# Kernel tuning notes

Hardware: AMD Instinct MI355X
Metric: run time of the kernel (lower is better)

Reference implementation:

```python
import jax, jax.numpy as jnp
import numpy as np
from jax import lax

EPS = 1e-5
T, N, E = 10, 10000, 320000
C_IN, C_HID, C_OUT = 16, 32, 16


def _stgcn_layer(x, edge_index, edge_weight, tw, tb, gw, gb, gamma, beta):
    # x: [T, N, Cin] -> temporal conv over T per node
    xc = jnp.transpose(x, (1, 2, 0))  # [N, Cin, T]
    y = lax.conv_general_dilated(xc, tw, window_strides=(1,), padding=((1, 1),),
                                 dimension_numbers=("NCH", "OIH", "NCH"))
    y = y + tb[None, :, None]
    y = jnp.clip(y, -10.0, 10.0)
    # InstanceNorm1d (affine, biased var over time axis)
    mu = jnp.mean(y, axis=-1, keepdims=True)
    var = jnp.mean((y - mu) ** 2, axis=-1, keepdims=True)
    y = (y - mu) * lax.rsqrt(var + EPS) * gamma[None, :, None] + beta[None, :, None]
    y = jax.nn.relu(y)
    h = jnp.transpose(y, (0, 2, 1))  # [N, T, C]

    n = h.shape[0]
    # GCNConv normalization (identical at every timestep -> computed once)
    ewn = jax.nn.softmax(edge_weight)  # softmax over all E edges
    loop = jnp.arange(n, dtype=edge_index.dtype)
    row = jnp.concatenate([edge_index[0], loop])  # sources (+self loops)
    col = jnp.concatenate([edge_index[1], loop])  # destinations
    w = jnp.concatenate([ewn, jnp.ones((n,), dtype=ewn.dtype)])
    deg = jax.ops.segment_sum(w, col, num_segments=n)
    dinv = jnp.where(deg > 0, lax.rsqrt(jnp.maximum(deg, EPS * 0 + 1e-30)), 0.0)
    norm = dinv[row] * w * dinv[col]  # [E+N]

    hw = jnp.einsum("ntc,cd->ntd", h, gw)  # [N, T, C]
    msg = hw[row] * norm[:, None, None]     # [E+N, T, C] gather
    agg = jax.ops.segment_sum(msg, col, num_segments=n) + gb  # scatter-add
    out = jnp.clip(jax.nn.relu(agg), -10.0, 10.0)
    return jnp.transpose(out, (1, 0, 2))  # [T, N, C]


def setup_inputs() -> dict:
    key = jax.random.key(0)
    ks = jax.random.split(key, 16)
    inp = {
        "x": jax.random.normal(ks[0], (T, N, C_IN), dtype=jnp.float32),
        "edge_index": jax.random.randint(ks[1], (2, E), 0, N, dtype=jnp.int32),
        "edge_weight": jax.random.uniform(ks[2], (E,), dtype=jnp.float32),
        # layer 1 (in -> hid)
        "l1_tw": jax.random.normal(ks[3], (C_HID, C_IN, 3), dtype=jnp.float32) * 0.02,
        "l1_tb": jnp.zeros((C_HID,), dtype=jnp.float32),
        "l1_gw": jax.random.normal(ks[4], (C_HID, C_HID), dtype=jnp.float32) * 0.1,
        "l1_gb": jnp.zeros((C_HID,), dtype=jnp.float32),
        "l1_gamma": jnp.ones((C_HID,), dtype=jnp.float32),
        "l1_beta": jnp.zeros((C_HID,), dtype=jnp.float32),
        # layer 2 (hid -> hid)
        "l2_tw": jax.random.normal(ks[5], (C_HID, C_HID, 3), dtype=jnp.float32) * 0.02,
        "l2_tb": jnp.zeros((C_HID,), dtype=jnp.float32),
        "l2_gw": jax.random.normal(ks[6], (C_HID, C_HID), dtype=jnp.float32) * 0.1,
        "l2_gb": jnp.zeros((C_HID,), dtype=jnp.float32),
        "l2_gamma": jnp.ones((C_HID,), dtype=jnp.float32),
        "l2_beta": jnp.zeros((C_HID,), dtype=jnp.float32),
        # output linear
        "out_w": jax.random.normal(ks[7], (C_HID, C_OUT), dtype=jnp.float32) * 0.1,
        "out_b": jnp.zeros((C_OUT,), dtype=jnp.float32),
    }
    return inp


def reference(x, edge_index, edge_weight,
              l1_tw, l1_tb, l1_gw, l1_gb, l1_gamma, l1_beta,
              l2_tw, l2_tb, l2_gw, l2_gb, l2_gamma, l2_beta,
              out_w, out_b):
    h = _stgcn_layer(x, edge_index, edge_weight, l1_tw, l1_tb, l1_gw, l1_gb, l1_gamma, l1_beta)
    h = _stgcn_layer(h, edge_index, edge_weight, l2_tw, l2_tb, l2_gw, l2_gb, l2_gamma, l2_beta)
    # per-timestep linear then mean over time == mean then linear, done faithfully
    outs = jnp.einsum("tnc,cd->tnd", h, out_w) + out_b
    return jnp.mean(outs, axis=0)  # [N, C_OUT]
```

## Files before the change

kernel.cpp:

```cpp
#include <hip/hip_runtime.h>
#include <hip/hip_bf16.h>
#include <string.h>


typedef __hip_bfloat16 bf16;

#define TSTEPS 10
#define TPAD 12
#define CHID 32
#define ROWELE (TSTEPS * CHID)
#define ROWW4 40

__device__ __forceinline__ float b2f(bf16 v) { return __bfloat162float(v); }
__device__ __forceinline__ float ldf(const void* p, long i, int bf) {
    return bf ? __bfloat162float(((const bf16*)p)[i]) : ((const float*)p)[i];
}
__device__ __forceinline__ int detect_bf(const unsigned* gbits) {
    return (gbits[0] != 0x3F800000u) ? 1 : 0;
}
__device__ __forceinline__ float bflo(unsigned u) { return __uint_as_float(u << 16); }
__device__ __forceinline__ float bfhi(unsigned u) { return __uint_as_float(u & 0xFFFF0000u); }
__device__ __forceinline__ unsigned pack2bf(float a, float b) {
    bf16 x = __float2bfloat16(a), y = __float2bfloat16(b);
    unsigned short ux, uy;
    memcpy(&ux, &x, 2); memcpy(&uy, &y, 2);
    return (unsigned)ux | ((unsigned)uy << 16);
}
__device__ __forceinline__ unsigned short bfbits(float a) {
    bf16 x = __float2bfloat16(a);
    unsigned short u; memcpy(&u, &x, 2);
    return u;
}
__device__ __forceinline__ void accum8(float* f, uint4 u, float w) {
    f[0] += w * bflo(u.x); f[1] += w * bfhi(u.x);
    f[2] += w * bflo(u.y); f[3] += w * bfhi(u.y);
    f[4] += w * bflo(u.z); f[5] += w * bfhi(u.z);
    f[6] += w * bflo(u.w); f[7] += w * bfhi(u.w);
}


__device__ __forceinline__ void edge_body(
    int bb, const void* __restrict__ ew, int bf, const int* __restrict__ ei,
    float* __restrict__ ewn, float* __restrict__ degx, int* __restrict__ cnt,
    float* __restrict__ sumexp, int E, int tid) {
    __shared__ float s_red[4];
    int i0 = (bb * 256 + tid) * 4;
    float e0 = 0.0f, e1 = 0.0f, e2 = 0.0f, e3 = 0.0f;
    if ((E & 3) == 0 && i0 + 3 < E) {
        float w0, w1, w2, w3;
        if (bf) {
            uint2 u = ((const uint2*)ew)[i0 >> 2];
            w0 = bflo(u.x); w1 = bfhi(u.x); w2 = bflo(u.y); w3 = bfhi(u.y);
        } else {
            float4 f = ((const float4*)ew)[i0 >> 2];
            w0 = f.x; w1 = f.y; w2 = f.z; w3 = f.w;
        }
        e0 = __expf(w0); e1 = __expf(w1); e2 = __expf(w2); e3 = __expf(w3);
        int4 c4 = *(const int4*)&ei[E + i0];
        atomicAdd(&degx[c4.x], e0); atomicAdd(&cnt[c4.x], 1);
        atomicAdd(&degx[c4.y], e1); atomicAdd(&cnt[c4.y], 1);
        atomicAdd(&degx[c4.z], e2); atomicAdd(&cnt[c4.z], 1);
        atomicAdd(&degx[c4.w], e3); atomicAdd(&cnt[c4.w], 1);
        *(float4*)&ewn[i0] = make_float4(e0, e1, e2, e3);
    } else {
        float es[4] = {0, 0, 0, 0};
        for (int j = 0; j < 4; j++) {
            int i = i0 + j;
            if (i < E) {
                float e = __expf(ldf(ew, i, bf));
                es[j] = e;
                ewn[i] = e;
                int c = ei[E + i];
                atomicAdd(&degx[c], e);
                atomicAdd(&cnt[c], 1);
            }
        }
        e0 = es[0]; e1 = es[1]; e2 = es[2]; e3 = es[3];
    }
    float v = (e0 + e1) + (e2 + e3);
    for (int o = 32; o > 0; o >>= 1) v += __shfl_down(v, o);
    int lane = tid & 63, wv = tid >> 6;
    if (lane == 0) s_red[wv] = v;
    __syncthreads();
    if (tid == 0) atomicAdd(sumexp, s_red[0] + s_red[1] + s_red[2] + s_red[3]);
}


template <int CIN, int LAYOUT>
__device__ __forceinline__ void conv_body(
    int bb, const void* __restrict__ in_, int bfw,
    const void* __restrict__ tw, const void* __restrict__ tb,
    const void* __restrict__ gamma, const void* __restrict__ beta,
    const void* __restrict__ gw,
    bf16* __restrict__ hw, int N, int tid) {
    constexpr int CO = CHID;
    __shared__ __align__(16) float s_in[8 * CIN * TPAD];
    __shared__ __align__(16) float s_h[8 * CO * TPAD];
    __shared__ __align__(16) unsigned s_tw01[CIN * CO];
    __shared__ __align__(16) unsigned short s_tw2[CIN * CO];
    __shared__ __align__(16) unsigned s_gwp[(CO / 2) * CO];

    int nl = tid >> 5, o = tid & 31;

    float tbv = ldf(tb, o, bfw);
    float gav = ldf(gamma, o, bfw);
    float bev = ldf(beta, o, bfw);

    for (int i = tid; i < CIN * CO; i += 256) {
        int ci = i / CO, oo = i % CO;
        long base = ((long)oo * CIN + ci) * 3;
        float w0 = ldf(tw, base, bfw);
        float w1 = ldf(tw, base + 1, bfw);
        float w2 = ldf(tw, base + 2, bfw);
        s_tw01[ci * CO + oo] = pack2bf(w0, w1);
        s_tw2[ci * CO + oo] = bfbits(w2);
    }
    for (int i = tid; i < (CO / 2) * CO; i += 256) {
        int cp = i / CO, oo = i % CO;
        s_gwp[i] = pack2bf(ldf(gw, (long)(2 * cp) * CO + oo, bfw),
                           ldf(gw, (long)(2 * cp + 1) * CO + oo, bfw));
    }

    int nb = bb * 8;

    if (LAYOUT == 0) {
        constexpr int CP = CIN / 2;
        for (int i2 = tid; i2 < 8 * TSTEPS * CP; i2 += 256) {
            int cp = i2 % CP;
            int t = (i2 / CP) % TSTEPS;
            int nn = i2 / (CP * TSTEPS);
            int n = nb + nn;
            float v0 = 0.0f, v1 = 0.0f;
            if (n < N) {
                long idx = (long)t * ((long)N * CIN) + (long)n * CIN + 2 * cp;
                if (bfw) {
                    unsigned u = ((const unsigned*)in_)[idx >> 1];
                    v0 = bflo(u); v1 = bfhi(u);
                } else {
                    float2 f = ((const float2*)in_)[idx >> 1];
                    v0 = f.x; v1 = f.y;
                }
            }
            int b = nn * (CIN * TPAD) + (2 * cp) * TPAD + t;
            s_in[b] = v0;
            s_in[b + TPAD] = v1;
        }
    } else {
        for (int i2 = tid; i2 < 8 * CIN * 5; i2 += 256) {
            int tp = i2 % 5;
            int ci = (i2 / 5) % CIN;
            int nn = i2 / (5 * CIN);
            int n = nb + nn;
            float v0 = 0.0f, v1 = 0.0f;
            if (n < N) {
                long idx = (long)n * (CIN * TSTEPS) + ci * TSTEPS + 2 * tp;
                unsigned u = ((const unsigned*)in_)[idx >> 1];
                v0 = bflo(u); v1 = bfhi(u);
            }
            int b = nn * (CIN * TPAD) + ci * TPAD + 2 * tp;
            s_in[b] = v0;
            s_in[b + 1] = v1;
        }
    }
    __syncthreads();

    int n = nb + nl;
    const float* xrow = &s_in[nl * CIN * TPAD];

    float acc[TSTEPS];
#pragma unroll
    for (int t = 0; t < TSTEPS; t++) acc[t] = tbv;

    for (int ci = 0; ci < CIN; ci++) {
        const float4* xp = (const float4*)&xrow[ci * TPAD];
        float4 A = xp[0], B = xp[1], C = xp[2];
        float xr[TSTEPS] = {A.x, A.y, A.z, A.w, B.x, B.y, B.z, B.w, C.x, C.y};
        unsigned w01 = s_tw01[ci * CO + o];
        float w0 = bflo(w01), w1 = bfhi(w01);
        float w2 = __uint_as_float(((unsigned)s_tw2[ci * CO + o]) << 16);
        acc[0] += xr[0] * w1 + xr[1] * w2;
#pragma unroll
        for (int t = 1; t < TSTEPS - 1; t++)
            acc[t] += xr[t - 1] * w0 + xr[t] * w1 + xr[t + 1] * w2;
        acc[TSTEPS - 1] += xr[TSTEPS - 2] * w0 + xr[TSTEPS - 1] * w1;
    }

#pragma unroll
    for (int t = 0; t < TSTEPS; t++) acc[t] = fminf(fmaxf(acc[t], -10.0f), 10.0f);
    float mu = 0.0f;
#pragma unroll
    for (int t = 0; t < TSTEPS; t++) mu += acc[t];
    mu *= 0.1f;
    float var = 0.0f;
#pragma unroll
    for (int t = 0; t < TSTEPS; t++) { float d = acc[t] - mu; var += d * d; }
    var *= 0.1f;
    float sc = gav * rsqrtf(var + 1e-5f);
    float h[TSTEPS];
#pragma unroll
    for (int t = 0; t < TSTEPS; t++) h[t] = fmaxf((acc[t] - mu) * sc + bev, 0.0f);

    float4* hp = (float4*)&s_h[nl * CO * TPAD + o * TPAD];
    hp[0] = make_float4(h[0], h[1], h[2], h[3]);
    hp[1] = make_float4(h[4], h[5], h[6], h[7]);
    hp[2] = make_float4(h[8], h[9], 0.0f, 0.0f);
    __syncthreads();

    float acc2[TSTEPS];
#pragma unroll
    for (int t = 0; t < TSTEPS; t++) acc2[t] = 0.0f;
    const float* hrow = &s_h[nl * CO * TPAD];
    for (int cp = 0; cp < CO / 2; cp++) {
        unsigned g2 = s_gwp[cp * CO + o];
        float g0 = bflo(g2), g1 = bfhi(g2);
        const float4* r0 = (const float4*)&hrow[(2 * cp) * TPAD];
        const float4* r1 = (const float4*)&hrow[(2 * cp + 1) * TPAD];
        float4 A0 = r0[0], B0 = r0[1], C0 = r0[2];
        float4 A1 = r1[0], B1 = r1[1], C1 = r1[2];
        acc2[0] += A0.x * g0 + A1.x * g1;
        acc2[1] += A0.y * g0 + A1.y * g1;
        acc2[2] += A0.z * g0 + A1.z * g1;
        acc2[3] += A0.w * g0 + A1.w * g1;
        acc2[4] += B0.x * g0 + B1.x * g1;
        acc2[5] += B0.y * g0 + B1.y * g1;
        acc2[6] += B0.z * g0 + B1.z * g1;
        acc2[7] += B0.w * g0 + B1.w * g1;
        acc2[8] += C0.x * g0 + C1.x * g1;
        acc2[9] += C0.y * g0 + C1.y * g1;
    }
    if (n < N) {
        unsigned* hwp = (unsigned*)hw;
        long base = (long)n * (ROWELE / 2) + o * (TSTEPS / 2);
#pragma unroll
        for (int j = 0; j < 5; j++)
            hwp[base + j] = pack2bf(acc2[2 * j], acc2[2 * j + 1]);
    }
}


__global__ __launch_bounds__(256) void edge_conv1_kernel(
    const void* __restrict__ ew, const unsigned* __restrict__ gbits,
    const int* __restrict__ ei,
    float* __restrict__ ewn, float* __restrict__ degx, int* __restrict__ cnt,
    float* __restrict__ sumexp, int E, int gE4,
    const void* __restrict__ x,
    const void* __restrict__ tw, const void* __restrict__ tb,
    const void* __restrict__ gamma, const void* __restrict__ beta,
    const void* __restrict__ gw,
    bf16* __restrict__ hw, int N) {
    int bf = detect_bf(gbits);
    int tid = threadIdx.x;
    if ((int)blockIdx.x < gE4) {
        edge_body(blockIdx.x, ew, bf, ei, ewn, degx, cnt, sumexp, E, tid);
    } else {
        conv_body<16, 0>(blockIdx.x - gE4, x, bf, tw, tb, gamma, beta, gw,
                         hw, N, tid);
    }
}

__global__ __launch_bounds__(256) void conv2_kernel(
    const void* __restrict__ in_, const unsigned* __restrict__ gbits,
    const void* __restrict__ tw, const void* __restrict__ tb,
    const void* __restrict__ gamma, const void* __restrict__ beta,
    const void* __restrict__ gw,
    bf16* __restrict__ hw, int N) {
    conv_body<32, 1>(blockIdx.x, in_, detect_bf(gbits), tw, tb, gamma, beta,
                     gw, hw, N, threadIdx.x);
}

__global__ __launch_bounds__(1024) void scan_kernel(const int* __restrict__ cnt,
                                                    const float* __restrict__ degx,
                                                    const float* __restrict__ sumexp,
                                                    float* __restrict__ dinv,
                                                    int* __restrict__ off, int N) {
    __shared__ int s[1024];
    int tid = threadIdx.x;
    float invS = 1.0f / (*sumexp);
    for (int i = tid; i < N; i += 1024) dinv[i] = rsqrtf(1.0f + degx[i] * invS);
    int chunk = (N + 1023) / 1024;
    int b0 = tid * chunk;
    int p = 0;
    for (int k = 0; k < chunk; k++) { int i = b0 + k; if (i < N) p += cnt[i]; }
    s[tid] = p;
    __syncthreads();
    for (int d = 1; d < 1024; d <<= 1) {
        int v = (tid >= d) ? s[tid - d] : 0;
        __syncthreads();
        s[tid] += v;
        __syncthreads();
    }
    int base = s[tid] - p;
    for (int k = 0; k < chunk; k++) {
        int i = b0 + k;
        if (i < N) {
            off[i] = base;
            base += cnt[i];
            if (i == N - 1) off[N] = base;
        }
    }
}


__global__ __launch_bounds__(256) void fill_kernel(const int* __restrict__ ei,
                                                   const float* __restrict__ ewn,
                                                   const float* __restrict__ dinv,
                                                   const float* __restrict__ sumexp,
                                                   const int* __restrict__ off,
                                                   int* __restrict__ cursor,
                                                   int2* __restrict__ csr, int E) {
    int i0 = (blockIdx.x * 256 + threadIdx.x) * 4;
    if (i0 >= E) return;
    float invS = 1.0f / (*sumexp);
    if ((E & 3) == 0 && i0 + 3 < E) {
        int4 r4 = *(const int4*)&ei[i0];
        int4 c4 = *(const int4*)&ei[E + i0];
        float4 e4 = *(const float4*)&ewn[i0];
        int rr[4] = {r4.x, r4.y, r4.z, r4.w};
        int cc[4] = {c4.x, c4.y, c4.z, c4.w};
        float ee[4] = {e4.x, e4.y, e4.z, e4.w};
#pragma unroll
        for (int j = 0; j < 4; j++) {
            int r = rr[j], c = cc[j];
            int p = atomicAdd(&cursor[c], 1);
            float w = dinv[r] * (ee[j] * invS) * dinv[c];
            csr[off[c] + p] = make_int2(r, __float_as_int(w));
        }
    } else {
        for (int j = 0; j < 4; j++) {
            int i = i0 + j;
            if (i >= E) break;
            int r = ei[i], c = ei[E + i];
            int p = atomicAdd(&cursor[c], 1);
            float w = dinv[r] * (ewn[i] * invS) * dinv[c];
            csr[off[c] + p] = make_int2(r, __float_as_int(w));
        }
    }
}


template <bool FINAL>
__global__ __launch_bounds__(320) void agg_kernel_t(
    const uint4* __restrict__ hw4, const int* __restrict__ off,
    const int2* __restrict__ csr,
    const float* __restrict__ dinv, const void* __restrict__ gb,
    const void* __restrict__ ow, const void* __restrict__ ob,
    const unsigned* __restrict__ gbits,
    void* __restrict__ out, int N) {
    __shared__ int2 s_sw[ROWELE];
    __shared__ float s_part[8 * ROWW4 * 9];
    __shared__ float s_hbar[CHID];
    __shared__ float s_ow[CHID * 16];
    __shared__ float s_ob[16];

    int bf = detect_bf(gbits);
    int n = blockIdx.x;
    int tid = threadIdx.x;
    int g = tid % ROWW4;
    int eo = tid / ROWW4;

    if (FINAL) {
        for (int i = tid; i < CHID * 16; i += ROWELE) s_ow[i] = ldf(ow, i, bf);
        if (tid < 16) s_ob[tid] = ldf(ob, tid, bf);
    }

    float facc[8];
#pragma unroll
    for (int j = 0; j < 8; j++) facc[j] = 0.0f;

    float dn = dinv[n];
    if (eo == 0) {
        uint4 u = hw4[n * ROWW4 + g];
        accum8(facc, u, dn * dn);
    }

    int beg = off[n], end = off[n + 1];
    for (int base = beg; base < end; base += ROWELE) {
        int m = min(ROWELE, end - base);
        if (tid < m) s_sw[tid] = csr[base + tid];
        __syncthreads();
        int kmax = (m + 7) >> 3;
        int k = 0;
        for (; k + 2 <= kmax; k += 2) {
            int j0 = (k << 3) + eo, j1 = j0 + 8;
            int c0 = min(j0, m - 1), c1 = min(j1, m - 1);
            int2 e0 = s_sw[c0], e1 = s_sw[c1];
            float w0 = (j0 < m) ? __int_as_float(e0.y) : 0.0f;
            float w1 = (j1 < m) ? __int_as_float(e1.y) : 0.0f;
            uint4 u0 = hw4[e0.x * ROWW4 + g];
            uint4 u1 = hw4[e1.x * ROWW4 + g];
            accum8(facc, u0, w0);
            accum8(facc, u1, w1);
        }
        if (k < kmax) {
            int j0 = (k << 3) + eo;
            int c0 = min(j0, m - 1);
            int2 e0 = s_sw[c0];
            float w0 = (j0 < m) ? __int_as_float(e0.y) : 0.0f;
            uint4 u0 = hw4[e0.x * ROWW4 + g];
            accum8(facc, u0, w0);
        }
        __syncthreads();
    }

    {
        float* rowp = &s_part[(eo * ROWW4 + g) * 9];
#pragma unroll
        for (int j = 0; j < 8; j++) rowp[j] = facc[j];
    }
    __syncthreads();
    int gg = tid >> 3, jj = tid & 7;
    float v = 0.0f;
#pragma unroll
    for (int s = 0; s < 8; s++) v += s_part[(s * ROWW4 + gg) * 9 + jj];
    int c = tid / TSTEPS;
    v += ldf(gb, c, bf);
    v = fminf(fmaxf(v, 0.0f), 10.0f);

    if (!FINAL) {
        ((bf16*)out)[(long)n * ROWELE + tid] = __float2bfloat16(v);
    } else {
        __syncthreads();
        s_part[tid] = v;
        __syncthreads();
        if (tid < CHID) {
            float s = 0.0f;
#pragma unroll
            for (int t = 0; t < TSTEPS; t++) s += s_part[tid * TSTEPS + t];
            s_hbar[tid] = s * 0.1f;
        }
        __syncthreads();
        if (tid < 16) {
            float a = s_ob[tid];
#pragma unroll
            for (int cc = 0; cc < CHID; cc++) a += s_hbar[cc] * s_ow[cc * 16 + tid];
            long oi = (long)n * 16 + tid;
            if (bf) ((bf16*)out)[oi] = __float2bfloat16(a);
            else    ((float*)out)[oi] = a;
        }
    }
}


extern "C" void kernel_launch(void* const* d_in, const int* in_sizes, int n_in,
                              void* d_out, int out_size, void* d_ws, size_t ws_size,
                              hipStream_t stream) {
    (void)n_in; (void)out_size; (void)ws_size;

    const void* x     = d_in[0];
    const int*  ei    = (const int*)d_in[1];
    const void* ew    = d_in[2];
    const void* l1_tw = d_in[3];
    const void* l1_tb = d_in[4];
    const void* l1_gw = d_in[5];
    const void* l1_gb = d_in[6];
    const unsigned* gbits = (const unsigned*)d_in[7];
    const void* l1_ga = d_in[7];
    const void* l1_be = d_in[8];
    const void* l2_tw = d_in[9];
    const void* l2_tb = d_in[10];
    const void* l2_gw = d_in[11];
    const void* l2_gb = d_in[12];
    const void* l2_ga = d_in[13];
    const void* l2_be = d_in[14];
    const void* out_w = d_in[15];
    const void* out_b = d_in[16];

    int N = in_sizes[0] / (TSTEPS * 16);
    int E = in_sizes[1] / 2;

    char* p = (char*)d_ws;
    auto alloc = [&](size_t bytes) -> char* {
        char* r = p;
        p += (bytes + 255) & ~(size_t)255;
        return r;
    };
    char* zbase   = p;
    float* sumexp = (float*)alloc(256);
    float* degx   = (float*)alloc((size_t)N * 4);
    int*   cnt    = (int*)alloc((size_t)N * 4);
    int*   cursor = (int*)alloc((size_t)N * 4);
    size_t zbytes = (size_t)(p - zbase);
    float* ewn     = (float*)alloc((size_t)E * 4);
    float* dinv    = (float*)alloc((size_t)N * 4);
    int*   offA    = (int*)alloc((size_t)(N + 1) * 4);
    int2*  csr     = (int2*)alloc((size_t)E * 8);
    bf16*  bufA    = (bf16*)alloc((size_t)N * ROWELE * 2);
    bf16*  bufB    = (bf16*)alloc((size_t)N * ROWELE * 2);

    int gE4 = (E + 1023) / 1024;
    int gConv = (N + 7) / 8;

    hipMemsetAsync(zbase, 0, zbytes, stream);
    hipLaunchKernelGGL(edge_conv1_kernel, dim3(gE4 + gConv), dim3(256), 0, stream,
                       ew, gbits, ei, ewn, degx, cnt, sumexp, E, gE4,
                       x, l1_tw, l1_tb, l1_ga, l1_be, l1_gw, bufA, N);
    hipLaunchKernelGGL(scan_kernel, dim3(1), dim3(1024), 0, stream,
                       cnt, degx, sumexp, dinv, offA, N);
    hipLaunchKernelGGL(fill_kernel, dim3(gE4), dim3(256), 0, stream,
                       ei, ewn, dinv, sumexp, offA, cursor, csr, E);

    hipLaunchKernelGGL((agg_kernel_t<false>), dim3(N), dim3(ROWELE), 0, stream,
                       (const uint4*)bufA, offA, csr, dinv, l1_gb,
                       nullptr, nullptr, gbits, (void*)bufB, N);
    hipLaunchKernelGGL(conv2_kernel, dim3(gConv), dim3(256), 0, stream,
                       (const void*)bufB, gbits, l2_tw, l2_tb, l2_ga, l2_be,
                       l2_gw, bufA, N);
    hipLaunchKernelGGL((agg_kernel_t<true>), dim3(N), dim3(ROWELE), 0, stream,
                       (const uint4*)bufA, offA, csr, dinv, l2_gb,
                       out_w, out_b, gbits, d_out, N);
}
```

Before: 278.6 us.

## Fuse scan into last edge block and layer-2 conv into first aggregation

The separate single-block scan kernel is removed. The last-finishing edge block, detected with an atomic done counter and threadfences, now computes dinv and the CSR offsets with a 256-thread scan. The layer-1 aggregation and the layer-2 temporal conv, instance norm and GCN weight multiply are fused into one per-node kernel, so the intermediate bufB round trip and two launches go away. In exchange, every node block reloads the conv weights into shared memory, the fused kernel uses more shared memory, and the scan now runs on 256 threads instead of 1024.

New measurement: 538.7 us. 93.3% more time.

```diff
diff --git a/kernel.cpp b/kernel.cpp
--- a/kernel.cpp
+++ b/kernel.cpp
@@ -11,7 +11,6 @@
 #define ROWELE (TSTEPS * CHID)
 #define ROWW4 40
 
-__device__ __forceinline__ float b2f(bf16 v) { return __bfloat162float(v); }
 __device__ __forceinline__ float ldf(const void* p, long i, int bf) {
     return bf ? __bfloat162float(((const bf16*)p)[i]) : ((const float*)p)[i];
 }
@@ -42,8 +41,11 @@
 __device__ __forceinline__ void edge_body(
     int bb, const void* __restrict__ ew, int bf, const int* __restrict__ ei,
     float* __restrict__ ewn, float* __restrict__ degx, int* __restrict__ cnt,
-    float* __restrict__ sumexp, int E, int tid) {
+    float* __restrict__ sumexp, int E, int gE4, int* __restrict__ done,
+    float* __restrict__ dinv, int* __restrict__ off, int N, int tid) {
     __shared__ float s_red[4];
+    __shared__ int s_last;
+    __shared__ int s_scan[256];
     int i0 = (bb * 256 + tid) * 4;
     float e0 = 0.0f, e1 = 0.0f, e2 = 0.0f, e3 = 0.0f;
     if ((E & 3) == 0 && i0 + 3 < E) {
@@ -83,6 +85,41 @@
     if (lane == 0) s_red[wv] = v;
     __syncthreads();
     if (tid == 0) atomicAdd(sumexp, s_red[0] + s_red[1] + s_red[2] + s_red[3]);
+
+    __threadfence();
+    __syncthreads();
+    if (tid == 0) s_last = (atomicAdd(done, 1) == gE4 - 1) ? 1 : 0;
+    __syncthreads();
+    if (!s_last) return;
+
+    __threadfence();
+    float invS = 1.0f / atomicAdd(sumexp, 0.0f);
+    for (int i = tid; i < N; i += 256)
+        dinv[i] = rsqrtf(1.0f + atomicAdd(&degx[i], 0.0f) * invS);
+    int chunk = (N + 255) >> 8;
+    int b0 = tid * chunk;
+    int p = 0;
+    for (int k = 0; k < chunk; k++) {
+        int i = b0 + k;
+        if (i < N) p += atomicAdd(&cnt[i], 0);
+    }
+    s_scan[tid] = p;
+    __syncthreads();
+    for (int d = 1; d < 256; d <<= 1) {
+        int u = (tid >= d) ? s_scan[tid - d] : 0;
+        __syncthreads();
+        s_scan[tid] += u;
+        __syncthreads();
+    }
+    int base = s_scan[tid] - p;
+    for (int k = 0; k < chunk; k++) {
+        int i = b0 + k;
+        if (i < N) {
+            off[i] = base;
+            base += atomicAdd(&cnt[i], 0);
+            if (i == N - 1) off[N] = base;
+        }
+    }
 }
 
 
@@ -109,11 +146,8 @@
     for (int i = tid; i < CIN * CO; i += 256) {
         int ci = i / CO, oo = i % CO;
         long base = ((long)oo * CIN + ci) * 3;
-        float w0 = ldf(tw, base, bfw);
-        float w1 = ldf(tw, base + 1, bfw);
-        float w2 = ldf(tw, base + 2, bfw);
-        s_tw01[ci * CO + oo] = pack2bf(w0, w1);
-        s_tw2[ci * CO + oo] = bfbits(w2);
+        s_tw01[ci * CO + oo] = pack2bf(ldf(tw, base, bfw), ldf(tw, base + 1, bfw));
+        s_tw2[ci * CO + oo] = bfbits(ldf(tw, base + 2, bfw));
     }
     for (int i = tid; i < (CO / 2) * CO; i += 256) {
         int cp = i / CO, oo = i % CO;
@@ -122,45 +156,26 @@
     }
 
     int nb = bb * 8;
-
-    if (LAYOUT == 0) {
-        constexpr int CP = CIN / 2;
-        for (int i2 = tid; i2 < 8 * TSTEPS * CP; i2 += 256) {
-            int cp = i2 % CP;
-            int t = (i2 / CP) % TSTEPS;
-            int nn = i2 / (CP * TSTEPS);
-            int n = nb + nn;
-            float v0 = 0.0f, v1 = 0.0f;
-            if (n < N) {
-                long idx = (long)t * ((long)N * CIN) + (long)n * CIN + 2 * cp;
-                if (bfw) {
-                    unsigned u = ((const unsigned*)in_)[idx >> 1];
-                    v0 = bflo(u); v1 = bfhi(u);
-                } else {
-                    float2 f = ((const float2*)in_)[idx >> 1];
-                    v0 = f.x; v1 = f.y;
-                }
-            }
-            int b = nn * (CIN * TPAD) + (2 * cp) * TPAD + t;
-            s_in[b] = v0;
-            s_in[b + TPAD] = v1;
-        }
-    } else {
-        for (int i2 = tid; i2 < 8 * CIN * 5; i2 += 256) {
-            int tp = i2 % 5;
-            int ci = (i2 / 5) % CIN;
-            int nn = i2 / (5 * CIN);
-            int n = nb + nn;
-            float v0 = 0.0f, v1 = 0.0f;
-            if (n < N) {
-                long idx = (long)n * (CIN * TSTEPS) + ci * TSTEPS + 2 * tp;
+    constexpr int CP = CIN / 2;
+    for (int i2 = tid; i2 < 8 * TSTEPS * CP; i2 += 256) {
+        int cp = i2 % CP;
+        int t = (i2 / CP) % TSTEPS;
+        int nn = i2 / (CP * TSTEPS);
+        int n = nb + nn;
+        float v0 = 0.0f, v1 = 0.0f;
+        if (n < N) {
+            long idx = (long)t * ((long)N * CIN) + (long)n * CIN + 2 * cp;
+            if (bfw) {
                 unsigned u = ((const unsigned*)in_)[idx >> 1];
                 v0 = bflo(u); v1 = bfhi(u);
+            } else {
+                float2 f = ((const float2*)in_)[idx >> 1];
+                v0 = f.x; v1 = f.y;
             }
-            int b = nn * (CIN * TPAD) + ci * TPAD + 2 * tp;
-            s_in[b] = v0;
-            s_in[b + 1] = v1;
-        }
+        }
+        int b = nn * (CIN * TPAD) + (2 * cp) * TPAD + t;
+        s_in[b] = v0;
+        s_in[b + TPAD] = v1;
     }
     __syncthreads();
 
@@ -237,12 +252,12 @@
     }
 }
 
-
 __global__ __launch_bounds__(256) void edge_conv1_kernel(
     const void* __restrict__ ew, const unsigned* __restrict__ gbits,
     const int* __restrict__ ei,
     float* __restrict__ ewn, float* __restrict__ degx, int* __restrict__ cnt,
-    float* __restrict__ sumexp, int E, int gE4,
+    float* __restrict__ sumexp, int E, int gE4, int* __restrict__ done,
+    float* __restrict__ dinv, int* __restrict__ off,
     const void* __restrict__ x,
     const void* __restrict__ tw, const void* __restrict__ tb,
     const void* __restrict__ gamma, const void* __restrict__ beta,
@@ -251,55 +266,13 @@
     int bf = detect_bf(gbits);
     int tid = threadIdx.x;
     if ((int)blockIdx.x < gE4) {
-        edge_body(blockIdx.x, ew, bf, ei, ewn, degx, cnt, sumexp, E, tid);
+        edge_body(blockIdx.x, ew, bf, ei, ewn, degx, cnt, sumexp, E, gE4,
+                  done, dinv, off, N, tid);
     } else {
         conv_body<16, 0>(blockIdx.x - gE4, x, bf, tw, tb, gamma, beta, gw,
                          hw, N, tid);
     }
 }
-
-__global__ __launch_bounds__(256) void conv2_kernel(
-    const void* __restrict__ in_, const unsigned* __restrict__ gbits,
-    const void* __restrict__ tw, const void* __restrict__ tb,
-    const void* __restrict__ gamma, const void* __restrict__ beta,
-    const void* __restrict__ gw,
-    bf16* __restrict__ hw, int N) {
-    conv_body<32, 1>(blockIdx.x, in_, detect_bf(gbits), tw, tb, gamma, beta,
-                     gw, hw, N, threadIdx.x);
-}
-
-__global__ __launch_bounds__(1024) void scan_kernel(const int* __restrict__ cnt,
-                                                    const float* __restrict__ degx,
-                                                    const float* __restrict__ sumexp,
-                                                    float* __restrict__ dinv,
-                                                    int* __restrict__ off, int N) {
-    __shared__ int s[1024];
-    int tid = threadIdx.x;
-    float invS = 1.0f / (*sumexp);
-    for (int i = tid; i < N; i += 1024) dinv[i] = rsqrtf(1.0f + degx[i] * invS);
-    int chunk = (N + 1023) / 1024;
-    int b0 = tid * chunk;
-    int p = 0;
-    for (int k = 0; k < chunk; k++) { int i = b0 + k; if (i < N) p += cnt[i]; }
-    s[tid] = p;
-    __syncthreads();
-    for (int d = 1; d < 1024; d <<= 1) {
-        int v = (tid >= d) ? s[tid - d] : 0;
-        __syncthreads();
-        s[tid] += v;
-        __syncthreads();
-    }
-    int base = s[tid] - p;
-    for (int k = 0; k < chunk; k++) {
-        int i = b0 + k;
-        if (i < N) {
-            off[i] = base;
-            base += cnt[i];
-            if (i == N - 1) off[N] = base;
-        }
-    }
-}
-
 
 __global__ __launch_bounds__(256) void fill_kernel(const int* __restrict__ ei,
                                                    const float* __restrict__ ewn,
@@ -338,30 +311,13 @@
 }
 
 
-template <bool FINAL>
-__global__ __launch_bounds__(320) void agg_kernel_t(
-    const uint4* __restrict__ hw4, const int* __restrict__ off,
-    const int2* __restrict__ csr,
-    const float* __restrict__ dinv, const void* __restrict__ gb,
-    const void* __restrict__ ow, const void* __restrict__ ob,
-    const unsigned* __restrict__ gbits,
-    void* __restrict__ out, int N) {
-    __shared__ int2 s_sw[ROWELE];
-    __shared__ float s_part[8 * ROWW4 * 9];
-    __shared__ float s_hbar[CHID];
-    __shared__ float s_ow[CHID * 16];
-    __shared__ float s_ob[16];
-
-    int bf = detect_bf(gbits);
-    int n = blockIdx.x;
-    int tid = threadIdx.x;
+__device__ __forceinline__ float agg_gather(
+    int n, int tid, const uint4* __restrict__ hw4, const int* __restrict__ off,
+    const int2* __restrict__ csr, const float* __restrict__ dinv,
+    const void* __restrict__ gb, int bf,
+    int2* s_sw, float* s_part) {
     int g = tid % ROWW4;
     int eo = tid / ROWW4;
-
-    if (FINAL) {
-        for (int i = tid; i < CHID * 16; i += ROWELE) s_ow[i] = ldf(ow, i, bf);
-        if (tid < 16) s_ob[tid] = ldf(ob, tid, bf);
-    }
 
     float facc[8];
 #pragma unroll
@@ -414,29 +370,157 @@
     for (int s = 0; s < 8; s++) v += s_part[(s * ROWW4 + gg) * 9 + jj];
     int c = tid / TSTEPS;
     v += ldf(gb, c, bf);
-    v = fminf(fmaxf(v, 0.0f), 10.0f);
-
-    if (!FINAL) {
-        ((bf16*)out)[(long)n * ROWELE + tid] = __float2bfloat16(v);
-    } else {
-        __syncthreads();
-        s_part[tid] = v;
-        __syncthreads();
-        if (tid < CHID) {
-            float s = 0.0f;
-#pragma unroll
-            for (int t = 0; t < TSTEPS; t++) s += s_part[tid * TSTEPS + t];
-            s_hbar[tid] = s * 0.1f;
-        }
-        __syncthreads();
-        if (tid < 16) {
-            float a = s_ob[tid];
-#pragma unroll
-            for (int cc = 0; cc < CHID; cc++) a += s_hbar[cc] * s_ow[cc * 16 + tid];
-            long oi = (long)n * 16 + tid;
-            if (bf) ((bf16*)out)[oi] = __float2bfloat16(a);
-            else    ((float*)out)[oi] = a;
-        }
+    return fminf(fmaxf(v, 0.0f), 10.0f);
+}
+
+
+__global__ __launch_bounds__(ROWELE) void agg1_conv2_kernel(
+    const uint4* __restrict__ hw4, const int* __restrict__ off,
+    const int2* __restrict__ csr,
+    const float* __restrict__ dinv, const void* __restrict__ gb,
+    const void* __restrict__ tw, const void* __restrict__ tb,
+    const void* __restrict__ gamma, const void* __restrict__ beta,
+    const void* __restrict__ gw,
+    const unsigned* __restrict__ gbits,
+    unsigned* __restrict__ hw2, int N) {
+    __shared__ int2 s_sw[ROWELE];
+    __shared__ float s_part[8 * ROWW4 * 9];
+    __shared__ float s_x[ROWELE];
+    __shared__ float s_y[ROWELE];
+    __shared__ float s_hh[ROWELE];
+    __shared__ unsigned s_tw01[CHID * CHID];
+    __shared__ unsigned short s_tw2[CHID * CHID];
+    __shared__ unsigned s_gwp[(CHID / 2) * CHID];
+    __shared__ float s_tb2[CHID], s_ga2[CHID], s_be2[CHID];
+    __shared__ float s_mu[CHID], s_sc[CHID];
+
+    int bf = detect_bf(gbits);
+    int n = blockIdx.x;
+    int tid = threadIdx.x;
+
+    for (int i = tid; i < CHID * CHID; i += ROWELE) {
+        int ci = i >> 5, o = i & 31;
+        long base = ((long)o * CHID + ci) * 3;
+        s_tw01[i] = pack2bf(ldf(tw, base, bf), ldf(tw, base + 1, bf));
+        s_tw2[i] = bfbits(ldf(tw, base + 2, bf));
+    }
+    for (int i = tid; i < (CHID / 2) * CHID; i += ROWELE) {
+        int cp = i >> 5, o = i & 31;
+        s_gwp[i] = pack2bf(ldf(gw, (long)(2 * cp) * CHID + o, bf),
+                           ldf(gw, (long)(2 * cp + 1) * CHID + o, bf));
+    }
+    if (tid < CHID) {
+        s_tb2[tid] = ldf(tb, tid, bf);
+        s_ga2[tid] = ldf(gamma, tid, bf);
+        s_be2[tid] = ldf(beta, tid, bf);
+    }
+
+    float v = agg_gather(n, tid, hw4, off, csr, dinv, gb, bf, s_sw, s_part);
+    s_x[tid] = v;
+    __syncthreads();
+
+    int o = tid / 5, j = tid % 5, t0 = 2 * j;
+    float y0 = 0.0f, y1 = 0.0f;
+    if (tid < 160) {
+        float a0 = s_tb2[o], a1 = a0;
+        for (int ci = 0; ci < CHID; ci++) {
+            const float* xb = &s_x[ci * TSTEPS];
+            float xm = (t0 > 0) ? xb[t0 - 1] : 0.0f;
+            float x0 = xb[t0];
+            float x1 = xb[t0 + 1];
+            float xp = (t0 < 8) ? xb[t0 + 2] : 0.0f;
+            unsigned w01 = s_tw01[ci * CHID + o];
+            float w0 = bflo(w01), w1 = bfhi(w01);
+            float w2 = __uint_as_float(((unsigned)s_tw2[ci * CHID + o]) << 16);
+            a0 += xm * w0 + x0 * w1 + x1 * w2;
+            a1 += x0 * w0 + x1 * w1 + xp * w2;
+        }
+        y0 = fminf(fmaxf(a0, -10.0f), 10.0f);
+        y1 = fminf(fmaxf(a1, -10.0f), 10.0f);
+        s_y[o * TSTEPS + t0] = y0;
+        s_y[o * TSTEPS + t0 + 1] = y1;
+    }
+    __syncthreads();
+
+    if (tid < CHID) {
+        const float* yb = &s_y[tid * TSTEPS];
+        float yv[TSTEPS];
+#pragma unroll
+        for (int t = 0; t < TSTEPS; t++) yv[t] = yb[t];
+        float mu = 0.0f;
+#pragma unroll
+        for (int t = 0; t < TSTEPS; t++) mu += yv[t];
+        mu *= 0.1f;
+        float var = 0.0f;
+#pragma unroll
+        for (int t = 0; t < TSTEPS; t++) { float d = yv[t] - mu; var += d * d; }
+        var *= 0.1f;
+        s_mu[tid] = mu;
+        s_sc[tid] = s_ga2[tid] * rsqrtf(var + 1e-5f);
+    }
+    __syncthreads();
+
+    if (tid < 160) {
+        float mu = s_mu[o], sc = s_sc[o], be = s_be2[o];
+        s_hh[o * TSTEPS + t0] = fmaxf((y0 - mu) * sc + be, 0.0f);
+        s_hh[o * TSTEPS + t0 + 1] = fmaxf((y1 - mu) * sc + be, 0.0f);
+    }
+    __syncthreads();
+
+    if (tid < 160) {
+        float a0 = 0.0f, a1 = 0.0f;
+        for (int cp = 0; cp < CHID / 2; cp++) {
+            unsigned g2 = s_gwp[cp * CHID + o];
+            float g0 = bflo(g2), g1 = bfhi(g2);
+            const float* h0 = &s_hh[(2 * cp) * TSTEPS];
+            const float* h1 = &s_hh[(2 * cp + 1) * TSTEPS];
+            a0 += h0[t0] * g0 + h1[t0] * g1;
+            a1 += h0[t0 + 1] * g0 + h1[t0 + 1] * g1;
+        }
+        hw2[(long)n * (ROWELE / 2) + tid] = pack2bf(a0, a1);
+    }
+}
+
+
+__global__ __launch_bounds__(ROWELE) void agg_final_kernel(
+    const uint4* __restrict__ hw4, const int* __restrict__ off,
+    const int2* __restrict__ csr,
+    const float* __restrict__ dinv, const void* __restrict__ gb,
+    const void* __restrict__ ow, const void* __restrict__ ob,
+    const unsigned* __restrict__ gbits,
+    void* __restrict__ out, int N) {
+    __shared__ int2 s_sw[ROWELE];
+    __shared__ float s_part[8 * ROWW4 * 9];
+    __shared__ float s_hbar[CHID];
+    __shared__ float s_ow[CHID * 16];
+    __shared__ float s_ob[16];
+
+    int bf = detect_bf(gbits);
+    int n = blockIdx.x;
+    int tid = threadIdx.x;
+
+    for (int i = tid; i < CHID * 16; i += ROWELE) s_ow[i] = ldf(ow, i, bf);
+    if (tid < 16) s_ob[tid] = ldf(ob, tid, bf);
+
+    float v = agg_gather(n, tid, hw4, off, csr, dinv, gb, bf, s_sw, s_part);
+
+    __syncthreads();
+    s_part[tid] = v;
+    __syncthreads();
+    if (tid < CHID) {
+        float s = 0.0f;
+#pragma unroll
+        for (int t = 0; t < TSTEPS; t++) s += s_part[tid * TSTEPS + t];
+        s_hbar[tid] = s * 0.1f;
+    }
+    __syncthreads();
+    if (tid < 16) {
+        float a = s_ob[tid];
+#pragma unroll
+        for (int cc = 0; cc < CHID; cc++) a += s_hbar[cc] * s_ow[cc * 16 + tid];
+        long oi = (long)n * 16 + tid;
+        if (bf) ((bf16*)out)[oi] = __float2bfloat16(a);
+        else    ((float*)out)[oi] = a;
     }
 }
 
@@ -475,7 +559,9 @@
         return r;
     };
     char* zbase   = p;
-    float* sumexp = (float*)alloc(256);
+    char* hdr     = alloc(256);
+    float* sumexp = (float*)hdr;
+    int*   done   = (int*)(hdr + 8);
     float* degx   = (float*)alloc((size_t)N * 4);
     int*   cnt    = (int*)alloc((size_t)N * 4);
     int*   cursor = (int*)alloc((size_t)N * 4);
@@ -493,19 +579,15 @@
     hipMemsetAsync(zbase, 0, zbytes, stream);
     hipLaunchKernelGGL(edge_conv1_kernel, dim3(gE4 + gConv), dim3(256), 0, stream,
                        ew, gbits, ei, ewn, degx, cnt, sumexp, E, gE4,
+                       done, dinv, offA,
                        x, l1_tw, l1_tb, l1_ga, l1_be, l1_gw, bufA, N);
-    hipLaunchKernelGGL(scan_kernel, dim3(1), dim3(1024), 0, stream,
-                       cnt, degx, sumexp, dinv, offA, N);
     hipLaunchKernelGGL(fill_kernel, dim3(gE4), dim3(256), 0, stream,
                        ei, ewn, dinv, sumexp, offA, cursor, csr, E);
-
-    hipLaunchKernelGGL((agg_kernel_t<false>), dim3(N), dim3(ROWELE), 0, stream,
+    hipLaunchKernelGGL(agg1_conv2_kernel, dim3(N), dim3(ROWELE), 0, stream,
                        (const uint4*)bufA, offA, csr, dinv, l1_gb,
-                       nullptr, nullptr, gbits, (void*)bufB, N);
-    hipLaunchKernelGGL(conv2_kernel, dim3(gConv), dim3(256), 0, stream,
-                       (const void*)bufB, gbits, l2_tw, l2_tb, l2_ga, l2_be,
-                       l2_gw, bufA, N);
-    hipLaunchKernelGGL((agg_kernel_t<true>), dim3(N), dim3(ROWELE), 0, stream,
-                       (const uint4*)bufA, offA, csr, dinv, l2_gb,
+                       l2_tw, l2_tb, l2_ga, l2_be, l2_gw, gbits,
+                       (unsigned*)bufB, N);
+    hipLaunchKernelGGL(agg_final_kernel, dim3(N), dim3(ROWELE), 0, stream,
+                       (const uint4*)bufB, offA, csr, dinv, l2_gb,
                        out_w, out_b, gbits, d_out, N);
 }
```

## Fuse degree scan into edge kernel via last-block pattern; unroll gather by four

Applied to the files above, without the earlier changes.

The separate single-block scan kernel is removed. The last edge block to finish, detected with an atomic done counter and thread fences, now computes dinv and the CSR offsets with a 256-thread scan. This saves one kernel launch, but the scan now runs on 256 threads inside one block, so it may be slower than the old 1024-thread version. Separately, the aggregation inner loop is unrolled from two to four gathered rows per iteration to put more loads in flight.

Result: slower. 312.6 us (+12.2%).

```diff
diff --git a/kernel.cpp b/kernel.cpp
--- a/kernel.cpp
+++ b/kernel.cpp
@@ -11,7 +11,6 @@
 #define ROWELE (TSTEPS * CHID)
 #define ROWW4 40
 
-__device__ __forceinline__ float b2f(bf16 v) { return __bfloat162float(v); }
 __device__ __forceinline__ float ldf(const void* p, long i, int bf) {
     return bf ? __bfloat162float(((const bf16*)p)[i]) : ((const float*)p)[i];
 }
@@ -42,8 +41,11 @@
 __device__ __forceinline__ void edge_body(
     int bb, const void* __restrict__ ew, int bf, const int* __restrict__ ei,
     float* __restrict__ ewn, float* __restrict__ degx, int* __restrict__ cnt,
-    float* __restrict__ sumexp, int E, int tid) {
+    float* __restrict__ sumexp, int E, int gE4, int* __restrict__ done,
+    float* __restrict__ dinv, int* __restrict__ off, int N, int tid) {
     __shared__ float s_red[4];
+    __shared__ int s_last;
+    __shared__ int s_scan[256];
     int i0 = (bb * 256 + tid) * 4;
     float e0 = 0.0f, e1 = 0.0f, e2 = 0.0f, e3 = 0.0f;
     if ((E & 3) == 0 && i0 + 3 < E) {
@@ -83,6 +85,41 @@
     if (lane == 0) s_red[wv] = v;
     __syncthreads();
     if (tid == 0) atomicAdd(sumexp, s_red[0] + s_red[1] + s_red[2] + s_red[3]);
+
+    __threadfence();
+    __syncthreads();
+    if (tid == 0) s_last = (atomicAdd(done, 1) == gE4 - 1) ? 1 : 0;
+    __syncthreads();
+    if (!s_last) return;
+
+    __threadfence();
+    float invS = 1.0f / atomicAdd(sumexp, 0.0f);
+    for (int i = tid; i < N; i += 256)
+        dinv[i] = rsqrtf(1.0f + atomicAdd(&degx[i], 0.0f) * invS);
+    int chunk = (N + 255) >> 8;
+    int b0 = tid * chunk;
+    int p = 0;
+    for (int k = 0; k < chunk; k++) {
+        int i = b0 + k;
+        if (i < N) p += atomicAdd(&cnt[i], 0);
+    }
+    s_scan[tid] = p;
+    __syncthreads();
+    for (int d = 1; d < 256; d <<= 1) {
+        int u = (tid >= d) ? s_scan[tid - d] : 0;
+        __syncthreads();
+        s_scan[tid] += u;
+        __syncthreads();
+    }
+    int base = s_scan[tid] - p;
+    for (int k = 0; k < chunk; k++) {
+        int i = b0 + k;
+        if (i < N) {
+            off[i] = base;
+            base += atomicAdd(&cnt[i], 0);
+            if (i == N - 1) off[N] = base;
+        }
+    }
 }
 
 
@@ -109,11 +146,8 @@
     for (int i = tid; i < CIN * CO; i += 256) {
         int ci = i / CO, oo = i % CO;
         long base = ((long)oo * CIN + ci) * 3;
-        float w0 = ldf(tw, base, bfw);
-        float w1 = ldf(tw, base + 1, bfw);
-        float w2 = ldf(tw, base + 2, bfw);
-        s_tw01[ci * CO + oo] = pack2bf(w0, w1);
-        s_tw2[ci * CO + oo] = bfbits(w2);
+        s_tw01[ci * CO + oo] = pack2bf(ldf(tw, base, bfw), ldf(tw, base + 1, bfw));
+        s_tw2[ci * CO + oo] = bfbits(ldf(tw, base + 2, bfw));
     }
     for (int i = tid; i < (CO / 2) * CO; i += 256) {
         int cp = i / CO, oo = i % CO;
@@ -122,7 +156,6 @@
     }
 
     int nb = bb * 8;
-
     if (LAYOUT == 0) {
         constexpr int CP = CIN / 2;
         for (int i2 = tid; i2 < 8 * TSTEPS * CP; i2 += 256) {
@@ -237,12 +270,12 @@
     }
 }
 
-
 __global__ __launch_bounds__(256) void edge_conv1_kernel(
     const void* __restrict__ ew, const unsigned* __restrict__ gbits,
     const int* __restrict__ ei,
     float* __restrict__ ewn, float* __restrict__ degx, int* __restrict__ cnt,
-    float* __restrict__ sumexp, int E, int gE4,
+    float* __restrict__ sumexp, int E, int gE4, int* __restrict__ done,
+    float* __restrict__ dinv, int* __restrict__ off,
     const void* __restrict__ x,
     const void* __restrict__ tw, const void* __restrict__ tb,
     const void* __restrict__ gamma, const void* __restrict__ beta,
@@ -251,7 +284,8 @@
     int bf = detect_bf(gbits);
     int tid = threadIdx.x;
     if ((int)blockIdx.x < gE4) {
-        edge_body(blockIdx.x, ew, bf, ei, ewn, degx, cnt, sumexp, E, tid);
+        edge_body(blockIdx.x, ew, bf, ei, ewn, degx, cnt, sumexp, E, gE4,
+                  done, dinv, off, N, tid);
     } else {
         conv_body<16, 0>(blockIdx.x - gE4, x, bf, tw, tb, gamma, beta, gw,
                          hw, N, tid);
@@ -267,39 +301,6 @@
     conv_body<32, 1>(blockIdx.x, in_, detect_bf(gbits), tw, tb, gamma, beta,
                      gw, hw, N, threadIdx.x);
 }
-
-__global__ __launch_bounds__(1024) void scan_kernel(const int* __restrict__ cnt,
-                                                    const float* __restrict__ degx,
-                                                    const float* __restrict__ sumexp,
-                                                    float* __restrict__ dinv,
-                                                    int* __restrict__ off, int N) {
-    __shared__ int s[1024];
-    int tid = threadIdx.x;
-    float invS = 1.0f / (*sumexp);
-    for (int i = tid; i < N; i += 1024) dinv[i] = rsqrtf(1.0f + degx[i] * invS);
-    int chunk = (N + 1023) / 1024;
-    int b0 = tid * chunk;
-    int p = 0;
-    for (int k = 0; k < chunk; k++) { int i = b0 + k; if (i < N) p += cnt[i]; }
-    s[tid] = p;
-    __syncthreads();
-    for (int d = 1; d < 1024; d <<= 1) {
-        int v = (tid >= d) ? s[tid - d] : 0;
-        __syncthreads();
-        s[tid] += v;
-        __syncthreads();
-    }
-    int base = s[tid] - p;
-    for (int k = 0; k < chunk; k++) {
-        int i = b0 + k;
-        if (i < N) {
-            off[i] = base;
-            base += cnt[i];
-            if (i == N - 1) off[N] = base;
-        }
-    }
-}
-
 
 __global__ __launch_bounds__(256) void fill_kernel(const int* __restrict__ ei,
                                                    const float* __restrict__ ewn,
@@ -380,18 +381,25 @@
         __syncthreads();
         int kmax = (m + 7) >> 3;
         int k = 0;
-        for (; k + 2 <= kmax; k += 2) {
-            int j0 = (k << 3) + eo, j1 = j0 + 8;
+        for (; k + 4 <= kmax; k += 4) {
+            int j0 = (k << 3) + eo, j1 = j0 + 8, j2 = j0 + 16, j3 = j0 + 24;
             int c0 = min(j0, m - 1), c1 = min(j1, m - 1);
-            int2 e0 = s_sw[c0], e1 = s_sw[c1];
+            int c2 = min(j2, m - 1), c3 = min(j3, m - 1);
+            int2 e0 = s_sw[c0], e1 = s_sw[c1], e2 = s_sw[c2], e3 = s_sw[c3];
             float w0 = (j0 < m) ? __int_as_float(e0.y) : 0.0f;
             float w1 = (j1 < m) ? __int_as_float(e1.y) : 0.0f;
+            float w2 = (j2 < m) ? __int_as_float(e2.y) : 0.0f;
+            float w3 = (j3 < m) ? __int_as_float(e3.y) : 0.0f;
             uint4 u0 = hw4[e0.x * ROWW4 + g];
             uint4 u1 = hw4[e1.x * ROWW4 + g];
+            uint4 u2 = hw4[e2.x * ROWW4 + g];
+            uint4 u3 = hw4[e3.x * ROWW4 + g];
             accum8(facc, u0, w0);
             accum8(facc, u1, w1);
-        }
-        if (k < kmax) {
+            accum8(facc, u2, w2);
+            accum8(facc, u3, w3);
+        }
+        for (; k < kmax; k++) {
             int j0 = (k << 3) + eo;
             int c0 = min(j0, m - 1);
             int2 e0 = s_sw[c0];
@@ -475,7 +483,9 @@
         return r;
     };
     char* zbase   = p;
-    float* sumexp = (float*)alloc(256);
+    char* hdr     = alloc(256);
+    float* sumexp = (float*)hdr;
+    int*   done   = (int*)(hdr + 8);
     float* degx   = (float*)alloc((size_t)N * 4);
     int*   cnt    = (int*)alloc((size_t)N * 4);
     int*   cursor = (int*)alloc((size_t)N * 4);
@@ -493,12 +503,10 @@
     hipMemsetAsync(zbase, 0, zbytes, stream);
     hipLaunchKernelGGL(edge_conv1_kernel, dim3(gE4 + gConv), dim3(256), 0, stream,
                        ew, gbits, ei, ewn, degx, cnt, sumexp, E, gE4,
+                       done, dinv, offA,
                        x, l1_tw, l1_tb, l1_ga, l1_be, l1_gw, bufA, N);
-    hipLaunchKernelGGL(scan_kernel, dim3(1), dim3(1024), 0, stream,
-                       cnt, degx, sumexp, dinv, offA, N);
     hipLaunchKernelGGL(fill_kernel, dim3(gE4), dim3(256), 0, stream,
                        ei, ewn, dinv, sumexp, offA, cursor, csr, E);
-
     hipLaunchKernelGGL((agg_kernel_t<false>), dim3(N), dim3(ROWELE), 0, stream,
                        (const uint4*)bufA, offA, csr, dinv, l1_gb,
                        nullptr, nullptr, gbits, (void*)bufB, N);
```
